# Kernel optimization log

Hardware: AMD Instinct MI355X
Metric: run time of the kernel (lower is better)

Reference implementation:

```python
import math
import jax, jax.numpy as jnp
import numpy as np

H = 1024
N2 = 32  # N // 2
L_LEN = 4096


def setup_inputs() -> dict:
    key = jax.random.key(0)
    k0, k1, k2 = jax.random.split(key, 3)
    log_dt = jax.random.uniform(k0, (H,), dtype=jnp.float32) * (
        math.log(0.1) - math.log(0.001)) + math.log(0.001)
    C_real = jax.random.normal(k1, (H, N2), dtype=jnp.float32)
    C_imag = jax.random.normal(k2, (H, N2), dtype=jnp.float32)
    log_A_real = jnp.log(0.5 * jnp.ones((H, N2), dtype=jnp.float32))
    A_imag = math.pi * jnp.tile(jnp.arange(N2, dtype=jnp.float32)[None, :], (H, 1))
    return {
        "log_dt": log_dt,
        "C_real": C_real,
        "C_imag": C_imag,
        "log_A_real": log_A_real,
        "A_imag": A_imag,
        "L": L_LEN,
    }


def reference(log_dt, C_real, C_imag, log_A_real, A_imag, L):
    dt = jnp.exp(log_dt)                                   # [H]
    A = -jnp.exp(log_A_real) + 1j * A_imag                 # [H, N2] complex
    dtA = A * dt[:, None]                                  # [H, N2]
    l = jnp.arange(L, dtype=jnp.float32)                   # [L]
    Kexp = jnp.exp(dtA[:, :, None] * l)                    # [H, N2, L] complex (Vandermonde)
    Ct = (C_real + 1j * C_imag) * (jnp.exp(dtA) - 1.0) / A  # [H, N2]
    K = 2.0 * jnp.einsum('hn,hnl->hl', Ct, Kexp).real      # [H, L]
    return K
```

## Files before the change

kernel.cpp:

```cpp
#include <hip/hip_runtime.h>


#define N2   32
#define LLEN 4096
#define BLK  256
#define CL   (LLEN / BLK)
#define NCH  8

typedef float v2f __attribute__((ext_vector_type(2)));

__global__ __launch_bounds__(BLK, 4) void s4d_kernel(
    const float* __restrict__ log_dt,
    const float* __restrict__ C_real,
    const float* __restrict__ C_imag,
    const float* __restrict__ log_A_real,
    const float* __restrict__ A_imag,
    float* __restrict__ out)
{
    const int h = blockIdx.x;
    const int t = threadIdx.x;

    __shared__ float4  sA[N2];
    __shared__ double  sTrev[N2];
    __shared__ float   sDr[N2];

    if (t < N2) {
        const int n = t;
        const float dt = __expf(log_dt[h]);
        const float aR = -__expf(log_A_real[h * N2 + n]);
        const float aI = A_imag[h * N2 + n];
        const float dR = aR * dt;
        const float dI = aI * dt;

        const double trev = (double)dI * 0.15915494309189535;

        double phz = trev; phz -= floor(phz);
        const float e1 = __expf(dR);
        const float zr = e1 * __builtin_amdgcn_cosf((float)phz);
        const float zi = e1 * __builtin_amdgcn_sinf((float)phz);

        const float inv = 1.0f / (aR * aR + aI * aI);
        const float nr  = zr - 1.0f;
        const float ni  = zi;
        const float qr  = (nr * aR + ni * aI) * inv;
        const float qi  = (ni * aR - nr * aI) * inv;

        const float c_r = C_real[h * N2 + n], c_i = C_imag[h * N2 + n];
        const float Ctr = c_r * qr - c_i * qi;
        const float Cti = c_r * qi + c_i * qr;

        double ph2 = trev * (double)BLK; ph2 -= floor(ph2);
        const float ew = __expf(dR * (float)BLK);
        const float wr = ew * __builtin_amdgcn_cosf((float)ph2);
        const float wi = ew * __builtin_amdgcn_sinf((float)ph2);

        sA[n]    = make_float4(Ctr, Cti, wr, wi);
        sTrev[n] = trev;
        sDr[n]   = dR * 1.4426950408889634f;
    }
    __syncthreads();

    v2f acc[CL];
#pragma unroll
    for (int j = 0; j < CL; ++j) acc[j] = (v2f){0.0f, 0.0f};

    const float  tf = (float)t;
    const double td = (double)t;

    for (int n0 = 0; n0 < N2; n0 += NCH) {
        v2f s[NCH], w[NCH], wc[NCH];

#pragma unroll
        for (int k = 0; k < NCH; ++k) {
            const int n = n0 + k;
            const float4 A = sA[n];
            w[k]  = (v2f){ A.z,  A.w };
            wc[k] = (v2f){-A.w,  A.z };

            const float er = __builtin_amdgcn_exp2f(sDr[n] * tf);
            double p = sTrev[n] * td; p -= floor(p);
            const float ph01 = (float)p;
            const float pr  = er * __builtin_amdgcn_cosf(ph01);
            const float pim = er * __builtin_amdgcn_sinf(ph01);
            s[k] = (v2f){ A.x * pr - A.y * pim,
                          A.x * pim + A.y * pr };
        }

#pragma unroll
        for (int j = 0; j < CL; ++j) {
#pragma unroll
            for (int k = 0; k < NCH; ++k) {
                acc[j] += s[k];
                const v2f sx = __builtin_shufflevector(s[k], s[k], 0, 0);
                const v2f sy = __builtin_shufflevector(s[k], s[k], 1, 1);
                s[k] = sx * w[k] + sy * wc[k];
            }
        }
    }

    float* __restrict__ o = out + (size_t)h * LLEN + t;
#pragma unroll
    for (int j = 0; j < CL; ++j) o[j * BLK] = 2.0f * acc[j].x;
}

extern "C" void kernel_launch(void* const* d_in, const int* in_sizes, int n_in,
                              void* d_out, int out_size, void* d_ws, size_t ws_size,
                              hipStream_t stream) {
    const float* log_dt     = (const float*)d_in[0];
    const float* C_real     = (const float*)d_in[1];
    const float* C_imag     = (const float*)d_in[2];
    const float* log_A_real = (const float*)d_in[3];
    const float* A_imag     = (const float*)d_in[4];
    float* out = (float*)d_out;

    const int H = in_sizes[0];
    s4d_kernel<<<dim3(H), dim3(BLK), 0, stream>>>(
        log_dt, C_real, C_imag, log_A_real, A_imag, out);
}
```

Baseline: 84.70 us.

## Use real second-order recurrence over mode pairs and float double-single phase

```diff
diff --git a/kernel.cpp b/kernel.cpp
--- a/kernel.cpp
+++ b/kernel.cpp
@@ -1,11 +1,12 @@
 #include <hip/hip_runtime.h>
 
 
-#define N2   32
-#define LLEN 4096
-#define BLK  256
-#define CL   (LLEN / BLK)
-#define NCH  8
+#define N2    32
+#define NPAIR (N2 / 2)
+#define LLEN  4096
+#define BLK   256
+#define CL    (LLEN / BLK)
+#define PCH   4
 
 typedef float v2f __attribute__((ext_vector_type(2)));
 
@@ -20,9 +21,14 @@
     const int h = blockIdx.x;
     const int t = threadIdx.x;
 
-    __shared__ float4  sA[N2];
-    __shared__ double  sTrev[N2];
-    __shared__ float   sDr[N2];
+    __shared__ v2f   sCt[N2];
+    __shared__ v2f   sW[N2];
+    __shared__ float sInvR2[N2];
+    __shared__ float s2A[N2];
+    __shared__ float sMR2[N2];
+    __shared__ float sDrL2[N2];
+    __shared__ float sTh[N2];
+    __shared__ float sTl[N2];
 
     if (t < N2) {
         const int n = t;
@@ -30,33 +36,39 @@
         const float aR = -__expf(log_A_real[h * N2 + n]);
         const float aI = A_imag[h * N2 + n];
         const float dR = aR * dt;
-        const float dI = aI * dt;
 
-        const double trev = (double)dI * 0.15915494309189535;
+        const double trev = (double)aI * (double)dt * 0.15915494309189535;
+        const float  th   = (float)trev;
+        const float  tl   = (float)(trev - (double)th);
 
-        double phz = trev; phz -= floor(phz);
+        double pz = trev; pz -= floor(pz);
         const float e1 = __expf(dR);
-        const float zr = e1 * __builtin_amdgcn_cosf((float)phz);
-        const float zi = e1 * __builtin_amdgcn_sinf((float)phz);
+        const float zr = e1 * __builtin_amdgcn_cosf((float)pz);
+        const float zi = e1 * __builtin_amdgcn_sinf((float)pz);
 
         const float inv = 1.0f / (aR * aR + aI * aI);
         const float nr  = zr - 1.0f;
-        const float ni  = zi;
-        const float qr  = (nr * aR + ni * aI) * inv;
-        const float qi  = (ni * aR - nr * aI) * inv;
+        const float qr  = (nr * aR + zi * aI) * inv;
+        const float qi  = (zi * aR - nr * aI) * inv;
 
         const float c_r = C_real[h * N2 + n], c_i = C_imag[h * N2 + n];
         const float Ctr = c_r * qr - c_i * qi;
         const float Cti = c_r * qi + c_i * qr;
 
-        double ph2 = trev * (double)BLK; ph2 -= floor(ph2);
-        const float ew = __expf(dR * (float)BLK);
-        const float wr = ew * __builtin_amdgcn_cosf((float)ph2);
-        const float wi = ew * __builtin_amdgcn_sinf((float)ph2);
+        double p256 = trev * 256.0; p256 -= floor(p256);
+        const float ew = __expf(dR * 256.0f);
+        const float wa = ew * __builtin_amdgcn_cosf((float)p256);
+        const float wb = ew * __builtin_amdgcn_sinf((float)p256);
+        const float r2 = ew * ew;
 
-        sA[n]    = make_float4(Ctr, Cti, wr, wi);
-        sTrev[n] = trev;
-        sDr[n]   = dR * 1.4426950408889634f;
+        sCt[n]    = (v2f){Ctr, Cti};
+        sW[n]     = (v2f){wa, wb};
+        sInvR2[n] = 1.0f / r2;
+        s2A[n]    = 2.0f * wa;
+        sMR2[n]   = -r2;
+        sDrL2[n]  = dR * 1.4426950408889634f;
+        sTh[n]    = th;
+        sTl[n]    = tl;
     }
     __syncthreads();
 
@@ -64,43 +76,56 @@
 #pragma unroll
     for (int j = 0; j < CL; ++j) acc[j] = (v2f){0.0f, 0.0f};
 
-    const float  tf = (float)t;
-    const double td = (double)t;
+    const float tf = (float)t;
+    const v2f* __restrict__ p2A  = (const v2f*)s2A;
+    const v2f* __restrict__ pMR2 = (const v2f*)sMR2;
 
-    for (int n0 = 0; n0 < N2; n0 += NCH) {
-        v2f s[NCH], w[NCH], wc[NCH];
+    for (int p0 = 0; p0 < NPAIR; p0 += PCH) {
+        v2f x[PCH], xm[PCH], c2a[PCH], cmr[PCH];
 
 #pragma unroll
-        for (int k = 0; k < NCH; ++k) {
-            const int n = n0 + k;
-            const float4 A = sA[n];
-            w[k]  = (v2f){ A.z,  A.w };
-            wc[k] = (v2f){-A.w,  A.z };
+        for (int k = 0; k < PCH; ++k) {
+            const int pair = p0 + k;
+            c2a[k] = p2A[pair];
+            cmr[k] = pMR2[pair];
 
-            const float er = __builtin_amdgcn_exp2f(sDr[n] * tf);
-            double p = sTrev[n] * td; p -= floor(p);
-            const float ph01 = (float)p;
-            const float pr  = er * __builtin_amdgcn_cosf(ph01);
-            const float pim = er * __builtin_amdgcn_sinf(ph01);
-            s[k] = (v2f){ A.x * pr - A.y * pim,
-                          A.x * pim + A.y * pr };
+#pragma unroll
+            for (int e = 0; e < 2; ++e) {
+                const int n = 2 * pair + e;
+                const float er = __builtin_amdgcn_exp2f(sDrL2[n] * tf);
+                const float th = sTh[n], tl = sTl[n];
+                const float p  = th * tf;
+                const float perr = __builtin_fmaf(th, tf, -p);
+                float f = __builtin_amdgcn_fractf(p);
+                f += __builtin_fmaf(tl, tf, perr);
+                const float c = __builtin_amdgcn_cosf(f);
+                const float s = __builtin_amdgcn_sinf(f);
+
+                const v2f Ct = sCt[n];
+                const v2f w  = sW[n];
+                const float x0 = er * (Ct.x * c - Ct.y * s);
+                const float y0 = er * (Ct.x * s + Ct.y * c);
+                const float xm1 = (x0 * w.x + y0 * w.y) * sInvR2[n];
+                if (e == 0) { x[k].x = x0; xm[k].x = xm1; }
+                else        { x[k].y = x0; xm[k].y = xm1; }
+            }
         }
 
 #pragma unroll
         for (int j = 0; j < CL; ++j) {
 #pragma unroll
-            for (int k = 0; k < NCH; ++k) {
-                acc[j] += s[k];
-                const v2f sx = __builtin_shufflevector(s[k], s[k], 0, 0);
-                const v2f sy = __builtin_shufflevector(s[k], s[k], 1, 1);
-                s[k] = sx * w[k] + sy * wc[k];
+            for (int k = 0; k < PCH; ++k) {
+                acc[j] += x[k];
+                const v2f tmp = cmr[k] * xm[k];
+                xm[k] = x[k];
+                x[k]  = c2a[k] * x[k] + tmp;
             }
         }
     }
 
     float* __restrict__ o = out + (size_t)h * LLEN + t;
 #pragma unroll
-    for (int j = 0; j < CL; ++j) o[j * BLK] = 2.0f * acc[j].x;
+    for (int j = 0; j < CL; ++j) o[j * BLK] = 2.0f * (acc[j].x + acc[j].y);
 }
 
 extern "C" void kernel_launch(void* const* d_in, const int* in_sizes, int n_in,
```

After: 80.14 us. -5.4%, faster.
